# Kernel optimization log

Measured on AMD Instinct MI355X. Metric: run time of the kernel, lower is better.

The kernel has to match this reference:

```python
import jax, jax.numpy as jnp
import numpy as np

B, T, D = 2, 2048, 1024
H = 16
HD = D // H  # 64


def _rope_tables(t_len, hd, dtype=jnp.float32):
    inv_freq = 1.0 / (10000.0 ** (jnp.arange(0, hd, 2, dtype=jnp.float32) / hd))
    freqs = jnp.outer(jnp.arange(t_len, dtype=jnp.float32), inv_freq)  # [T, hd/2]
    emb = jnp.concatenate([freqs, freqs], axis=-1)  # [T, hd]
    return emb.astype(dtype)


def _rotate_half(x):
    x1, x2 = jnp.split(x, 2, axis=-1)
    return jnp.concatenate([-x2, x1], axis=-1)


def setup_inputs() -> dict:
    key = jax.random.key(0)
    k1, k2, k3 = jax.random.split(key, 3)
    x = jax.random.normal(k1, (B, T, D), dtype=jnp.float32)
    w_qkv = jax.random.normal(k2, (D, 3 * D), dtype=jnp.float32) * (D ** -0.5)
    w_out = jax.random.normal(k3, (D, D), dtype=jnp.float32) * (D ** -0.5)
    return {"x": x, "w_qkv": w_qkv, "w_out": w_out}


def reference(x, w_qkv, w_out):
    Bc, Tc, Dc = x.shape
    scale = HD ** -0.5
    qkv = x @ w_qkv  # [B,T,3D]
    q, k, v = jnp.split(qkv, 3, axis=-1)
    # -> [B,H,T,hd]
    q = q.reshape(Bc, Tc, H, HD).transpose(0, 2, 1, 3)
    k = k.reshape(Bc, Tc, H, HD).transpose(0, 2, 1, 3)
    v = v.reshape(Bc, Tc, H, HD).transpose(0, 2, 1, 3)
    emb = _rope_tables(Tc, HD, x.dtype)  # [T,hd]
    cos = jnp.cos(emb)[None, None, :, :]
    sin = jnp.sin(emb)[None, None, :, :]
    q = q * cos + _rotate_half(q) * sin
    k = k * cos + _rotate_half(k) * sin
    attn = jnp.einsum('bhqd,bhkd->bhqk', q, k) * scale  # [B,H,T,T]
    causal = jnp.tril(jnp.ones((Tc, Tc), dtype=bool))
    attn = jnp.where(causal[None, None], attn, -jnp.inf)
    attn = jax.nn.softmax(attn, axis=-1)
    out = jnp.einsum('bhqk,bhkd->bhqd', attn, v)
    out = out.transpose(0, 2, 1, 3).reshape(Bc, Tc, Dc)
    return out @ w_out
```

## Files before the change

kernel.cpp:

```cpp
#include <hip/hip_runtime.h>

#define TSEQ 2048
#define DMODEL 1024
#define NHEAD 16
#define HDIM 64
#define NB 2
#define MROWS 4096
#define NQKV 3072
#define QSCALE 0.1803368801111204f
#define ROPE_C (13.2877123795494f / 32.0f)
#define NEGINF -3.0e38f

using s16x8 = __attribute__((ext_vector_type(8))) short;
using s16x4 = __attribute__((ext_vector_type(4))) short;
using f32x4 = __attribute__((ext_vector_type(4))) float;
using u32x2 = __attribute__((ext_vector_type(2))) unsigned int;

static __device__ __forceinline__ float b2f(unsigned short u) {
  union { unsigned int i; float f; } x; x.i = ((unsigned int)u) << 16; return x.f;
}
static __device__ __forceinline__ unsigned short f2b(float f) {
  unsigned int u = __float_as_uint(f);
  u += 0x7fffu + ((u >> 16) & 1u);
  return (unsigned short)(u >> 16);
}

typedef const __attribute__((address_space(1))) char gchar;
typedef __attribute__((address_space(3))) char lchar;
static __device__ __forceinline__ void gload_lds16(const void* g, void* l) {
  __builtin_amdgcn_global_load_lds((gchar*)g, (lchar*)l, 16, 0, 0);
}

__global__ __launch_bounds__(256) void k_prep(const float* __restrict__ x,
                                              short* __restrict__ xb,
                                              const float* __restrict__ wq,
                                              short* __restrict__ wqT,
                                              const float* __restrict__ wo,
                                              short* __restrict__ woT) {
  __shared__ float tile[32][33];
  const int blk = blockIdx.x;
  const int tid = threadIdx.x;
  if (blk < 4096) {
    const int i = blk * 256 + tid;
    const float4 v = ((const float4*)x)[i];
    s16x4 o;
    o.x = (short)f2b(v.x); o.y = (short)f2b(v.y);
    o.z = (short)f2b(v.z); o.w = (short)f2b(v.w);
    ((s16x4*)xb)[i] = o;
    return;
  }
  const float* in; short* out; int C, bx, by;
  if (blk < 7168) {
    const int l = blk - 4096; in = wq; out = wqT; C = NQKV;
    bx = l % 96; by = l / 96;
  } else {
    const int l = blk - 7168; in = wo; out = woT; C = DMODEL;
    bx = l & 31; by = l >> 5;
  }
  const int tx = tid & 31, ty4 = (tid >> 5) * 4;
#pragma unroll
  for (int i = 0; i < 4; ++i)
    tile[ty4 + i][tx] = in[(by * 32 + ty4 + i) * C + bx * 32 + tx];
  __syncthreads();
#pragma unroll
  for (int i = 0; i < 4; ++i)
    out[(bx * 32 + ty4 + i) * DMODEL + by * 32 + tx] = (short)f2b(tile[tx][ty4 + i]);
}

__global__ __launch_bounds__(256) void k_gemm_qkv(const short* __restrict__ A,
                                                  const short* __restrict__ BT,
                                                  short* __restrict__ Qo,
                                                  short* __restrict__ Ko,
                                                  short* __restrict__ Vt) {
  __shared__ __attribute__((aligned(16))) short As[128 * 32];
  __shared__ __attribute__((aligned(16))) short Bs[128 * 32];
  const int K = DMODEL, N = NQKV;
  const int tid = threadIdx.x;
  const int wave = tid >> 6, lane = tid & 63, quad = lane >> 4, l15 = lane & 15;
  const int wm = (wave >> 1) * 64, wn = (wave & 1) * 64;
  const int m0 = blockIdx.y * 128, n0 = blockIdx.x * 128;
  f32x4 acc[4][4] = {};
  const int r0 = tid >> 2, g0 = (tid & 3) ^ ((r0 >> 1) & 3);
  const int r1 = (tid + 256) >> 2, g1 = (tid & 3) ^ ((r1 >> 1) & 3);
  const char* Ab = (const char*)A;
  const char* Bb = (const char*)BT;
  char* AsB = (char*)As;
  char* BsB = (char*)Bs;
  const int ldsw0 = wave * 1024;
  const int ldsw1 = 4096 + wave * 1024;
  const long a0off = ((long)(m0 + r0) * K) * 2 + g0 * 16;
  const long a1off = ((long)(m0 + r1) * K) * 2 + g1 * 16;
  const long b0off = ((long)(n0 + r0) * K) * 2 + g0 * 16;
  const long b1off = ((long)(n0 + r1) * K) * 2 + g1 * 16;
  for (int k0 = 0; k0 < K; k0 += 32) {
    __syncthreads();
    gload_lds16(Ab + a0off + k0 * 2, AsB + ldsw0);
    gload_lds16(Ab + a1off + k0 * 2, AsB + ldsw1);
    gload_lds16(Bb + b0off + k0 * 2, BsB + ldsw0);
    gload_lds16(Bb + b1off + k0 * 2, BsB + ldsw1);
    __syncthreads();
    s16x8 af[4], bf[4];
#pragma unroll
    for (int i = 0; i < 4; ++i) {
      const int ra = wm + i * 16 + l15;
      af[i] = *(const s16x8*)(AsB + ra * 64 + ((quad ^ ((ra >> 1) & 3)) * 16));
      const int rb = wn + i * 16 + l15;
      bf[i] = *(const s16x8*)(BsB + rb * 64 + ((quad ^ ((rb >> 1) & 3)) * 16));
    }
#pragma unroll
    for (int i = 0; i < 4; ++i)
#pragma unroll
      for (int j = 0; j < 4; ++j)
        acc[i][j] = __builtin_amdgcn_mfma_f32_16x16x32_bf16(af[i], bf[j], acc[i][j], 0, 0, 0);
  }
  const int colbase = n0 + wn;
  const int region = colbase >> 10;
  const int hh = (colbase & 1023) >> 6;
  const int bq = m0 >> 11;
  const int tbase = (m0 & 2047) + wm;
  if (region == 2) {
    short* dst = Vt + (((long)(bq * NHEAD + hh) * HDIM) << 11);
#pragma unroll
    for (int i = 0; i < 4; ++i) {
      const int t0 = tbase + i * 16 + quad * 4;
#pragma unroll
      for (int j = 0; j < 4; ++j) {
        const int d = j * 16 + l15;
        s16x4 w;
        w.x = (short)f2b(acc[i][j][0]);
        w.y = (short)f2b(acc[i][j][1]);
        w.z = (short)f2b(acc[i][j][2]);
        w.w = (short)f2b(acc[i][j][3]);
        *(s16x4*)(dst + (((long)d) << 11) + t0) = w;
      }
    }
  } else {
    short* dst = (region ? Ko : Qo) + (long)(bq * NHEAD + hh) * TSEQ * HDIM;
    const float qs = region ? 1.0f : QSCALE;
    const float inv0 = exp2f(-(float)l15 * ROPE_C);
    const float inv1 = exp2f(-(float)(16 + l15) * ROPE_C);
#pragma unroll
    for (int i = 0; i < 4; ++i) {
#pragma unroll
      for (int r = 0; r < 4; ++r) {
        const int t = tbase + i * 16 + quad * 4 + r;
        float sn0, cs0, sn1, cs1;
        __sincosf((float)t * inv0, &sn0, &cs0);
        __sincosf((float)t * inv1, &sn1, &cs1);
        sn0 *= qs; cs0 *= qs; sn1 *= qs; cs1 *= qs;
        short* drow = dst + (long)t * HDIM;
        drow[l15]      = (short)f2b(acc[i][0][r] * cs0 - acc[i][2][r] * sn0);
        drow[16 + l15] = (short)f2b(acc[i][1][r] * cs1 - acc[i][3][r] * sn1);
        drow[32 + l15] = (short)f2b(acc[i][2][r] * cs0 + acc[i][0][r] * sn0);
        drow[48 + l15] = (short)f2b(acc[i][3][r] * cs1 + acc[i][1][r] * sn1);
      }
    }
  }
}

template <int IM, bool OUT_BF16>
__global__ __launch_bounds__(256) void k_gemm(const short* __restrict__ A,
                                              const short* __restrict__ BT,
                                              void* __restrict__ Cv,
                                              int M, int N, int K) {
  __shared__ __attribute__((aligned(16))) short As[IM * 32 * 32];
  __shared__ __attribute__((aligned(16))) short Bs[128 * 32];
  const int tid = threadIdx.x;
  const int wave = tid >> 6, lane = tid & 63, quad = lane >> 4, l15 = lane & 15;
  const int wm = (wave >> 1) * (IM * 16), wn = (wave & 1) * 64;
  const int m0 = blockIdx.y * (IM * 32), n0 = blockIdx.x * 128;
  f32x4 acc[IM][4] = {};
  const int r0 = tid >> 2, g0 = (tid & 3) ^ ((r0 >> 1) & 3);
  const int r1 = (tid + 256) >> 2, g1 = (tid & 3) ^ ((r1 >> 1) & 3);
  const char* Ab = (const char*)A;
  const char* Bb = (const char*)BT;
  char* AsB = (char*)As;
  char* BsB = (char*)Bs;
  const int ldsw0 = wave * 1024;
  const int ldsw1 = 4096 + wave * 1024;
  const long a0off = ((long)(m0 + r0) * K) * 2 + g0 * 16;
  const long a1off = ((long)(m0 + r1) * K) * 2 + g1 * 16;
  const long b0off = ((long)(n0 + r0) * K) * 2 + g0 * 16;
  const long b1off = ((long)(n0 + r1) * K) * 2 + g1 * 16;
  for (int k0 = 0; k0 < K; k0 += 32) {
    __syncthreads();
    gload_lds16(Ab + a0off + k0 * 2, AsB + ldsw0);
    if (IM == 4) gload_lds16(Ab + a1off + k0 * 2, AsB + ldsw1);
    gload_lds16(Bb + b0off + k0 * 2, BsB + ldsw0);
    gload_lds16(Bb + b1off + k0 * 2, BsB + ldsw1);
    __syncthreads();
    s16x8 af[IM], bf[4];
#pragma unroll
    for (int i = 0; i < IM; ++i) {
      const int ra = wm + i * 16 + l15;
      af[i] = *(const s16x8*)(AsB + ra * 64 + ((quad ^ ((ra >> 1) & 3)) * 16));
    }
#pragma unroll
    for (int j = 0; j < 4; ++j) {
      const int rb = wn + j * 16 + l15;
      bf[j] = *(const s16x8*)(BsB + rb * 64 + ((quad ^ ((rb >> 1) & 3)) * 16));
    }
#pragma unroll
    for (int i = 0; i < IM; ++i)
#pragma unroll
      for (int j = 0; j < 4; ++j)
        acc[i][j] = __builtin_amdgcn_mfma_f32_16x16x32_bf16(af[i], bf[j], acc[i][j], 0, 0, 0);
  }
#pragma unroll
  for (int i = 0; i < IM; ++i) {
    const int row = m0 + wm + i * 16 + quad * 4;
#pragma unroll
    for (int j = 0; j < 4; ++j) {
      const int col = n0 + wn + j * 16 + l15;
#pragma unroll
      for (int r = 0; r < 4; ++r) {
        if (OUT_BF16) ((short*)Cv)[(long)(row + r) * N + col] = (short)f2b(acc[i][j][r]);
        else          ((float*)Cv)[(long)(row + r) * N + col] = acc[i][j][r];
      }
    }
  }
}

__global__ __launch_bounds__(256) __attribute__((amdgpu_waves_per_eu(4)))
void k_attn(const short* __restrict__ Qg,
            const short* __restrict__ Kg,
            const short* __restrict__ Vg,
            short* __restrict__ O) {
  __shared__ __attribute__((aligned(16))) short Ks[2][64 * 64];
  __shared__ __attribute__((aligned(16))) short Vs[2][64 * 64];
  __shared__ __attribute__((aligned(16))) short pl[4][16 * 64];
  const int bx = blockIdx.x, by = blockIdx.y;
  const int r_ = (bx & 7) ^ (by & 7);
  const int idx_ = ((bx >> 3) + (by >> 3)) & 3;
  const int qi = (idx_ == 0) ? r_ : (idx_ == 1) ? 15 - r_ : (idx_ == 2) ? 16 + r_ : 31 - r_;
  const int bh = by;
  const int b = bh >> 4, h = bh & 15;
  const int tid = threadIdx.x, wave = tid >> 6, lane = tid & 63;
  const int quad = lane >> 4, l15 = lane & 15;
  const char* Kb = (const char*)(Kg + (long)bh * TSEQ * HDIM);
  const char* Vb = (const char*)(Vg + (long)bh * HDIM * TSEQ);
  const short* Qb = Qg + (long)bh * TSEQ * HDIM;
  const int qr0 = qi * 64 + wave * 16;
  const s16x8 aq0 = *(const s16x8*)&Qb[(qr0 + l15) * HDIM + quad * 8];
  const s16x8 aq1 = *(const s16x8*)&Qb[(qr0 + l15) * HDIM + 32 + quad * 8];
  f32x4 o[4] = {};
  float lsum = 0.0f;
  const int kr0 = tid >> 3, kg0 = (tid & 7) ^ (kr0 & 7);
  const int kr1 = (tid + 256) >> 3, kg1 = (tid & 7) ^ (kr1 & 7);
  char* KsB = (char*)Ks;
  char* VsB = (char*)Vs;
  char* plwB = (char*)pl + wave * 2048;
  const int ldsw0 = wave * 1024, ldsw1 = 4096 + wave * 1024;

#define STAGE(kjv, buf)                                                     \
  do {                                                                      \
    const char* Kt_ = Kb + (kjv) * 8192;                                    \
    const char* Vt_ = Vb + (kjv) * 128;                                     \
    char* kd_ = KsB + (buf) * 8192;                                         \
    char* vd_ = VsB + (buf) * 8192;                                         \
    gload_lds16(Kt_ + (kr0 * 8 + kg0) * 16, kd_ + ldsw0);                   \
    gload_lds16(Kt_ + (kr1 * 8 + kg1) * 16, kd_ + ldsw1);                   \
    gload_lds16(Vt_ + kr0 * (TSEQ * 2) + kg0 * 16, vd_ + ldsw0);            \
    gload_lds16(Vt_ + kr1 * (TSEQ * 2) + kg1 * 16, vd_ + ldsw1);            \
  } while (0)

  STAGE(0, 0);
  __syncthreads();

  for (int kj = 0; kj <= qi; ++kj) {
    const int cur = kj & 1;
    if (kj < qi) STAGE(kj + 1, cur ^ 1);
    const char* kb = KsB + cur * 8192;
    const char* vb = VsB + cur * 8192;

    f32x4 s[4];
#pragma unroll
    for (int j2 = 0; j2 < 4; ++j2) {
      const int row = j2 * 16 + l15;
      const s16x8 k0 = *(const s16x8*)(kb + row * 128 + ((quad ^ (row & 7)) * 16));
      const s16x8 k1 = *(const s16x8*)(kb + row * 128 + (((4 + quad) ^ (row & 7)) * 16));
      f32x4 z = {};
      z = __builtin_amdgcn_mfma_f32_16x16x32_bf16(k0, aq0, z, 0, 0, 0);
      z = __builtin_amdgcn_mfma_f32_16x16x32_bf16(k1, aq1, z, 0, 0, 0);
      s[j2] = z;
    }
    if (kj == qi) {
      const int q_loc = wave * 16 + l15;
#pragma unroll
      for (int j2 = 0; j2 < 4; ++j2)
#pragma unroll
        for (int r = 0; r < 4; ++r)
          if (j2 * 16 + quad * 4 + r > q_loc) s[j2][r] = NEGINF;
    }
    float ps = 0.0f;
#pragma unroll
    for (int j2 = 0; j2 < 4; ++j2) {
      const unsigned int u0 = __float_as_uint(exp2f(s[j2][0])) & 0xffff0000u;
      const unsigned int u1 = __float_as_uint(exp2f(s[j2][1])) & 0xffff0000u;
      const unsigned int u2 = __float_as_uint(exp2f(s[j2][2])) & 0xffff0000u;
      const unsigned int u3 = __float_as_uint(exp2f(s[j2][3])) & 0xffff0000u;
      ps += __uint_as_float(u0) + __uint_as_float(u1) +
            __uint_as_float(u2) + __uint_as_float(u3);
      u32x2 w;
      w.x = (u0 >> 16) | u1;
      w.y = (u2 >> 16) | u3;
      const int t0 = j2 * 16 + quad * 4;
      *(u32x2*)(plwB + l15 * 128 + (((t0 >> 3) ^ (l15 & 7)) * 16) + (quad & 1) * 8) = w;
    }
    lsum += ps;
    const s16x8 bp0 = *(const s16x8*)(plwB + l15 * 128 + ((quad ^ (l15 & 7)) * 16));
    const s16x8 bp1 = *(const s16x8*)(plwB + l15 * 128 + (((4 + quad) ^ (l15 & 7)) * 16));
#pragma unroll
    for (int hs = 0; hs < 4; ++hs) {
      const int d = hs * 16 + l15;
      const s16x8 av0 = *(const s16x8*)(vb + d * 128 + ((quad ^ (d & 7)) * 16));
      const s16x8 av1 = *(const s16x8*)(vb + d * 128 + (((4 + quad) ^ (d & 7)) * 16));
      o[hs] = __builtin_amdgcn_mfma_f32_16x16x32_bf16(av0, bp0, o[hs], 0, 0, 0);
      o[hs] = __builtin_amdgcn_mfma_f32_16x16x32_bf16(av1, bp1, o[hs], 0, 0, 0);
    }
    __syncthreads();
  }
#undef STAGE
  lsum += __shfl_xor(lsum, 16);
  lsum += __shfl_xor(lsum, 32);
  const float rinv = 1.0f / lsum;
  const int t = qi * 64 + wave * 16 + l15;
  short* Orow = O + (long)(b * TSEQ + t) * DMODEL + h * HDIM + quad * 4;
#pragma unroll
  for (int hs = 0; hs < 4; ++hs) {
    s16x4 w;
    w.x = (short)f2b(o[hs][0] * rinv);
    w.y = (short)f2b(o[hs][1] * rinv);
    w.z = (short)f2b(o[hs][2] * rinv);
    w.w = (short)f2b(o[hs][3] * rinv);
    *(s16x4*)(Orow + hs * 16) = w;
  }
}

extern "C" void kernel_launch(void* const* d_in, const int* in_sizes, int n_in,
                              void* d_out, int out_size, void* d_ws, size_t ws_size,
                              hipStream_t stream) {
  const float* x = (const float*)d_in[0];
  const float* w_qkv = (const float*)d_in[1];
  const float* w_out = (const float*)d_in[2];
  float* out = (float*)d_out;
  char* ws = (char*)d_ws;

  short* xb    = (short*)(ws);
  short* wqkvT = (short*)(ws + (8ll << 20));
  short* woutT = (short*)(ws + (14ll << 20));
  short* Qb    = (short*)(ws + (16ll << 20));
  short* Kb    = (short*)(ws + (24ll << 20));
  short* Vt    = (short*)(ws + (32ll << 20));
  short* Ob    = (short*)(ws + (40ll << 20));

  k_prep<<<dim3(8192), dim3(256), 0, stream>>>(x, xb, w_qkv, wqkvT, w_out, woutT);
  k_gemm_qkv<<<dim3(NQKV / 128, MROWS / 128), dim3(256), 0, stream>>>(
      xb, wqkvT, Qb, Kb, Vt);
  k_attn<<<dim3(TSEQ / 64, NB * NHEAD), dim3(256), 0, stream>>>(Qb, Kb, Vt, Ob);
  k_gemm<2, false><<<dim3(DMODEL / 128, MROWS / 64), dim3(256), 0, stream>>>(
      Ob, woutT, (void*)out, MROWS, DMODEL, DMODEL);
}
```

Measured before the change: 197.7 us.

## Move RoPE out of QKV GEMM epilogue into attention Q load and separate K kernel

The QKV GEMM epilogue now stores raw Q and K in bf16 without applying RoPE. K is rotated by a new standalone kernel that runs before attention, and Q is rotated and scaled inside the attention kernel when each wave loads its query fragment. The output projection GEMM tile also grows from 64 to 128 rows. The aim is to shorten the GEMM epilogue by removing its sincos work, at the cost of an extra launch and an extra read/write pass over K. Rotating bf16-rounded values instead of fp32 accumulators adds a second rounding step.

```diff
diff --git a/kernel.cpp b/kernel.cpp
--- a/kernel.cpp
+++ b/kernel.cpp
@@ -74,7 +74,7 @@
                                                   short* __restrict__ Vt) {
   __shared__ __attribute__((aligned(16))) short As[128 * 32];
   __shared__ __attribute__((aligned(16))) short Bs[128 * 32];
-  const int K = DMODEL, N = NQKV;
+  const int K = DMODEL;
   const int tid = threadIdx.x;
   const int wave = tid >> 6, lane = tid & 63, quad = lane >> 4, l15 = lane & 15;
   const int wm = (wave >> 1) * 64, wn = (wave & 1) * 64;
@@ -136,26 +136,42 @@
     }
   } else {
     short* dst = (region ? Ko : Qo) + (long)(bq * NHEAD + hh) * TSEQ * HDIM;
-    const float qs = region ? 1.0f : QSCALE;
-    const float inv0 = exp2f(-(float)l15 * ROPE_C);
-    const float inv1 = exp2f(-(float)(16 + l15) * ROPE_C);
-#pragma unroll
-    for (int i = 0; i < 4; ++i) {
-#pragma unroll
-      for (int r = 0; r < 4; ++r) {
-        const int t = tbase + i * 16 + quad * 4 + r;
-        float sn0, cs0, sn1, cs1;
-        __sincosf((float)t * inv0, &sn0, &cs0);
-        __sincosf((float)t * inv1, &sn1, &cs1);
-        sn0 *= qs; cs0 *= qs; sn1 *= qs; cs1 *= qs;
-        short* drow = dst + (long)t * HDIM;
-        drow[l15]      = (short)f2b(acc[i][0][r] * cs0 - acc[i][2][r] * sn0);
-        drow[16 + l15] = (short)f2b(acc[i][1][r] * cs1 - acc[i][3][r] * sn1);
-        drow[32 + l15] = (short)f2b(acc[i][2][r] * cs0 + acc[i][0][r] * sn0);
-        drow[48 + l15] = (short)f2b(acc[i][3][r] * cs1 + acc[i][1][r] * sn1);
+#pragma unroll
+    for (int i = 0; i < 4; ++i)
+#pragma unroll
+      for (int j = 0; j < 4; ++j) {
+        const int d = j * 16 + l15;
+#pragma unroll
+        for (int r = 0; r < 4; ++r) {
+          const int t = tbase + i * 16 + quad * 4 + r;
+          dst[(long)t * HDIM + d] = (short)f2b(acc[i][j][r]);
+        }
       }
-    }
-  }
+  }
+}
+
+__global__ __launch_bounds__(256) void k_ropek(short* __restrict__ Kp) {
+  const int tt = blockIdx.x, bh = blockIdx.y;
+  const int tid = threadIdx.x;
+  const int row = tid >> 2, chunk = tid & 3;
+  const int t = tt * 64 + row;
+  short* base = Kp + ((long)bh * TSEQ + t) * HDIM + chunk * 8;
+  const s16x8 lo = *(const s16x8*)base;
+  const s16x8 hi = *(const s16x8*)(base + 32);
+  s16x8 nlo, nhi;
+  const float tf = (float)t;
+#pragma unroll
+  for (int j = 0; j < 8; ++j) {
+    const float inv = exp2f(-(float)(chunk * 8 + j) * ROPE_C);
+    float sn, cs;
+    __sincosf(tf * inv, &sn, &cs);
+    const float a = b2f((unsigned short)lo[j]);
+    const float b = b2f((unsigned short)hi[j]);
+    nlo[j] = (short)f2b(a * cs - b * sn);
+    nhi[j] = (short)f2b(b * cs + a * sn);
+  }
+  *(s16x8*)base = nlo;
+  *(s16x8*)(base + 32) = nhi;
 }
 
 template <int IM, bool OUT_BF16>
@@ -241,8 +257,23 @@
   const char* Vb = (const char*)(Vg + (long)bh * HDIM * TSEQ);
   const short* Qb = Qg + (long)bh * TSEQ * HDIM;
   const int qr0 = qi * 64 + wave * 16;
-  const s16x8 aq0 = *(const s16x8*)&Qb[(qr0 + l15) * HDIM + quad * 8];
-  const s16x8 aq1 = *(const s16x8*)&Qb[(qr0 + l15) * HDIM + 32 + quad * 8];
+  const s16x8 rq0 = *(const s16x8*)&Qb[(qr0 + l15) * HDIM + quad * 8];
+  const s16x8 rq1 = *(const s16x8*)&Qb[(qr0 + l15) * HDIM + 32 + quad * 8];
+  s16x8 aq0, aq1;
+  {
+    const float tf = (float)(qr0 + l15);
+#pragma unroll
+    for (int j = 0; j < 8; ++j) {
+      const float inv = exp2f(-(float)(quad * 8 + j) * ROPE_C);
+      float sn, cs;
+      __sincosf(tf * inv, &sn, &cs);
+      sn *= QSCALE; cs *= QSCALE;
+      const float q0 = b2f((unsigned short)rq0[j]);
+      const float q1 = b2f((unsigned short)rq1[j]);
+      aq0[j] = (short)f2b(q0 * cs - q1 * sn);
+      aq1[j] = (short)f2b(q1 * cs + q0 * sn);
+    }
+  }
   f32x4 o[4] = {};
   float lsum = 0.0f;
   const int kr0 = tid >> 3, kg0 = (tid & 7) ^ (kr0 & 7);
@@ -357,7 +388,8 @@
   k_prep<<<dim3(8192), dim3(256), 0, stream>>>(x, xb, w_qkv, wqkvT, w_out, woutT);
   k_gemm_qkv<<<dim3(NQKV / 128, MROWS / 128), dim3(256), 0, stream>>>(
       xb, wqkvT, Qb, Kb, Vt);
+  k_ropek<<<dim3(TSEQ / 64, NB * NHEAD), dim3(256), 0, stream>>>(Kb);
   k_attn<<<dim3(TSEQ / 64, NB * NHEAD), dim3(256), 0, stream>>>(Qb, Kb, Vt, Ob);
-  k_gemm<2, false><<<dim3(DMODEL / 128, MROWS / 64), dim3(256), 0, stream>>>(
+  k_gemm<4, false><<<dim3(DMODEL / 128, MROWS / 128), dim3(256), 0, stream>>>(
       Ob, woutT, (void*)out, MROWS, DMODEL, DMODEL);
 }
```

New measurement: 212.3 us. 7.4% more time.
